# Optimization experiments

Measured on AMD Instinct MI355X. Metric: run time of the kernel, lower is better.

The kernel has to match this reference:

```python
import jax, jax.numpy as jnp
import numpy as np

N_ATOMS = 100000
N_EDGES = 6400000

def setup_inputs() -> dict:
    key = jax.random.key(0)
    k1, k2, k3 = jax.random.split(key, 3)
    R = jax.random.normal(k1, (N_ATOMS, 3), dtype=jnp.float32)
    idx_i = jax.random.randint(k2, (N_EDGES,), 0, N_ATOMS, dtype=jnp.int64)
    idx_j = jax.random.randint(k3, (N_EDGES,), 0, N_ATOMS, dtype=jnp.int64)
    return {"R": R, "idx_i": idx_i, "idx_j": idx_j}

def reference(R, idx_i, idx_j):
    # Gather coordinates at both ends of each edge, subtract, L2 norm over xyz.
    Rij = R[idx_i] - R[idx_j]            # [E, 3]
    d_ij = jnp.sqrt(jnp.sum(Rij * Rij, axis=-1))  # [E]
    return d_ij
```

## Files before the change

kernel.cpp:

```cpp
#include <hip/hip_runtime.h>
#include <hip/hip_bf16.h>


typedef int   v4i __attribute__((ext_vector_type(4)));
typedef float v4f __attribute__((ext_vector_type(4)));

__global__ __launch_bounds__(256) void pad_R_kernel(
    const float* __restrict__ R, float* __restrict__ R4, int n_atoms)
{
    const int i = blockIdx.x * blockDim.x + threadIdx.x;
    if (i < n_atoms) {
        const float x = R[3 * i + 0];
        const float y = R[3 * i + 1];
        const float z = R[3 * i + 2];
        v4f v = {x, y, z, 0.0f};
        *(v4f*)(R4 + 4 * (size_t)i) = v;
    }
}

__global__ __launch_bounds__(256) void pairwise_dist_kernel(
    const float* __restrict__ R4,
    const int* __restrict__ idx_i,
    const int* __restrict__ idx_j,
    float* __restrict__ out,
    int n_quads)
{
    const int quad = blockIdx.x * blockDim.x + threadIdx.x;
    if (quad >= n_quads) return;

    const v4i a = __builtin_nontemporal_load((const v4i*)idx_i + quad);
    const v4i b = __builtin_nontemporal_load((const v4i*)idx_j + quad);

    const v4f pa0 = __builtin_nontemporal_load((const v4f*)(R4 + 4 * (size_t)a.x));
    const v4f pb0 = __builtin_nontemporal_load((const v4f*)(R4 + 4 * (size_t)b.x));
    const v4f pa1 = __builtin_nontemporal_load((const v4f*)(R4 + 4 * (size_t)a.y));
    const v4f pb1 = __builtin_nontemporal_load((const v4f*)(R4 + 4 * (size_t)b.y));
    const v4f pa2 = __builtin_nontemporal_load((const v4f*)(R4 + 4 * (size_t)a.z));
    const v4f pb2 = __builtin_nontemporal_load((const v4f*)(R4 + 4 * (size_t)b.z));
    const v4f pa3 = __builtin_nontemporal_load((const v4f*)(R4 + 4 * (size_t)a.w));
    const v4f pb3 = __builtin_nontemporal_load((const v4f*)(R4 + 4 * (size_t)b.w));

    v4f o;
    {
        const v4f d = pa0 - pb0;
        o.x = sqrtf(d.x * d.x + d.y * d.y + d.z * d.z);
    }
    {
        const v4f d = pa1 - pb1;
        o.y = sqrtf(d.x * d.x + d.y * d.y + d.z * d.z);
    }
    {
        const v4f d = pa2 - pb2;
        o.z = sqrtf(d.x * d.x + d.y * d.y + d.z * d.z);
    }
    {
        const v4f d = pa3 - pb3;
        o.w = sqrtf(d.x * d.x + d.y * d.y + d.z * d.z);
    }
    __builtin_nontemporal_store(o, (v4f*)out + quad);
}

__global__ __launch_bounds__(64) void pairwise_dist_tail_kernel(
    const float* __restrict__ R4,
    const int* __restrict__ idx_i,
    const int* __restrict__ idx_j,
    float* __restrict__ out,
    int start, int n_edges)
{
    const int e = start + blockIdx.x * blockDim.x + threadIdx.x;
    if (e < n_edges) {
        const v4f pa = *(const v4f*)(R4 + 4 * (size_t)idx_i[e]);
        const v4f pb = *(const v4f*)(R4 + 4 * (size_t)idx_j[e]);
        const v4f d = pa - pb;
        out[e] = sqrtf(d.x * d.x + d.y * d.y + d.z * d.z);
    }
}

extern "C" void kernel_launch(void* const* d_in, const int* in_sizes, int n_in,
                              void* d_out, int out_size, void* d_ws, size_t ws_size,
                              hipStream_t stream)
{
    const float* R     = (const float*)d_in[0];
    const int*   idx_i = (const int*)d_in[1];
    const int*   idx_j = (const int*)d_in[2];
    float*       out   = (float*)d_out;

    const int n_atoms = in_sizes[0] / 3;
    const int n_edges = in_sizes[1];
    float*    R4      = (float*)d_ws;

    {
        const int block = 256;
        const int grid  = (n_atoms + block - 1) / block;
        pad_R_kernel<<<grid, block, 0, stream>>>(R, R4, n_atoms);
    }

    const int n_quads = n_edges >> 2;
    {
        const int block = 256;
        const int grid  = (n_quads + block - 1) / block;
        pairwise_dist_kernel<<<grid, block, 0, stream>>>(R4, idx_i, idx_j, out, n_quads);
    }

    const int tail_start = n_quads << 2;
    if (tail_start < n_edges) {
        const int tail = n_edges - tail_start;
        pairwise_dist_tail_kernel<<<(tail + 63) / 64, 64, 0, stream>>>(
            R4, idx_i, idx_j, out, tail_start, n_edges);
    }
}
```

Measured before the change: 159.5 us.

## Process eight edges per thread with inline-asm sc0 gathers and single wait

Each thread now handles eight edges instead of four, issuing sixteen coordinate gathers through inline global_load_dwordx4 with the sc0 cache-policy bit and then one explicit vmcnt(0) wait before computing distances. Index loads and output stores drop their nontemporal hints and become plain vector accesses. The aim is more memory-level parallelism per thread and keeping the small padded coordinate table cached rather than streamed. In exchange, register pressure rises, the thread count halves, and the hand-written asm hides the loads from compiler scheduling.

```diff
diff --git a/kernel.cpp b/kernel.cpp
--- a/kernel.cpp
+++ b/kernel.cpp
@@ -18,46 +18,67 @@
     }
 }
 
+__device__ __forceinline__ v4f gather_sc0(const float* base, int idx)
+{
+    v4f r;
+    const int voff = idx << 4;
+    asm volatile("global_load_dwordx4 %0, %1, %2 sc0"
+                 : "=v"(r)
+                 : "v"(voff), "s"(base)
+                 : "memory");
+    return r;
+}
+
+__device__ __forceinline__ float dist3(v4f a, v4f b)
+{
+    const v4f d = a - b;
+    return sqrtf(d.x * d.x + d.y * d.y + d.z * d.z);
+}
+
 __global__ __launch_bounds__(256) void pairwise_dist_kernel(
     const float* __restrict__ R4,
     const int* __restrict__ idx_i,
     const int* __restrict__ idx_j,
     float* __restrict__ out,
-    int n_quads)
+    int n_oct)
 {
-    const int quad = blockIdx.x * blockDim.x + threadIdx.x;
-    if (quad >= n_quads) return;
+    const int t = blockIdx.x * blockDim.x + threadIdx.x;
+    if (t >= n_oct) return;
 
-    const v4i a = __builtin_nontemporal_load((const v4i*)idx_i + quad);
-    const v4i b = __builtin_nontemporal_load((const v4i*)idx_j + quad);
+    const v4i a0 = ((const v4i*)idx_i)[2 * t + 0];
+    const v4i a1 = ((const v4i*)idx_i)[2 * t + 1];
+    const v4i b0 = ((const v4i*)idx_j)[2 * t + 0];
+    const v4i b1 = ((const v4i*)idx_j)[2 * t + 1];
 
-    const v4f pa0 = __builtin_nontemporal_load((const v4f*)(R4 + 4 * (size_t)a.x));
-    const v4f pb0 = __builtin_nontemporal_load((const v4f*)(R4 + 4 * (size_t)b.x));
-    const v4f pa1 = __builtin_nontemporal_load((const v4f*)(R4 + 4 * (size_t)a.y));
-    const v4f pb1 = __builtin_nontemporal_load((const v4f*)(R4 + 4 * (size_t)b.y));
-    const v4f pa2 = __builtin_nontemporal_load((const v4f*)(R4 + 4 * (size_t)a.z));
-    const v4f pb2 = __builtin_nontemporal_load((const v4f*)(R4 + 4 * (size_t)b.z));
-    const v4f pa3 = __builtin_nontemporal_load((const v4f*)(R4 + 4 * (size_t)a.w));
-    const v4f pb3 = __builtin_nontemporal_load((const v4f*)(R4 + 4 * (size_t)b.w));
+    v4f pa0 = gather_sc0(R4, a0.x), pb0 = gather_sc0(R4, b0.x);
+    v4f pa1 = gather_sc0(R4, a0.y), pb1 = gather_sc0(R4, b0.y);
+    v4f pa2 = gather_sc0(R4, a0.z), pb2 = gather_sc0(R4, b0.z);
+    v4f pa3 = gather_sc0(R4, a0.w), pb3 = gather_sc0(R4, b0.w);
+    v4f pa4 = gather_sc0(R4, a1.x), pb4 = gather_sc0(R4, b1.x);
+    v4f pa5 = gather_sc0(R4, a1.y), pb5 = gather_sc0(R4, b1.y);
+    v4f pa6 = gather_sc0(R4, a1.z), pb6 = gather_sc0(R4, b1.z);
+    v4f pa7 = gather_sc0(R4, a1.w), pb7 = gather_sc0(R4, b1.w);
 
-    v4f o;
-    {
-        const v4f d = pa0 - pb0;
-        o.x = sqrtf(d.x * d.x + d.y * d.y + d.z * d.z);
-    }
-    {
-        const v4f d = pa1 - pb1;
-        o.y = sqrtf(d.x * d.x + d.y * d.y + d.z * d.z);
-    }
-    {
-        const v4f d = pa2 - pb2;
-        o.z = sqrtf(d.x * d.x + d.y * d.y + d.z * d.z);
-    }
-    {
-        const v4f d = pa3 - pb3;
-        o.w = sqrtf(d.x * d.x + d.y * d.y + d.z * d.z);
-    }
-    __builtin_nontemporal_store(o, (v4f*)out + quad);
+    asm volatile("s_waitcnt vmcnt(0)"
+                 : "+v"(pa0), "+v"(pb0), "+v"(pa1), "+v"(pb1),
+                   "+v"(pa2), "+v"(pb2), "+v"(pa3), "+v"(pb3),
+                   "+v"(pa4), "+v"(pb4), "+v"(pa5), "+v"(pb5),
+                   "+v"(pa6), "+v"(pb6), "+v"(pa7), "+v"(pb7)
+                 :
+                 : "memory");
+
+    v4f o0, o1;
+    o0.x = dist3(pa0, pb0);
+    o0.y = dist3(pa1, pb1);
+    o0.z = dist3(pa2, pb2);
+    o0.w = dist3(pa3, pb3);
+    o1.x = dist3(pa4, pb4);
+    o1.y = dist3(pa5, pb5);
+    o1.z = dist3(pa6, pb6);
+    o1.w = dist3(pa7, pb7);
+
+    ((v4f*)out)[2 * t + 0] = o0;
+    ((v4f*)out)[2 * t + 1] = o1;
 }
 
 __global__ __launch_bounds__(64) void pairwise_dist_tail_kernel(
@@ -71,8 +92,7 @@
     if (e < n_edges) {
         const v4f pa = *(const v4f*)(R4 + 4 * (size_t)idx_i[e]);
         const v4f pb = *(const v4f*)(R4 + 4 * (size_t)idx_j[e]);
-        const v4f d = pa - pb;
-        out[e] = sqrtf(d.x * d.x + d.y * d.y + d.z * d.z);
+        out[e] = dist3(pa, pb);
     }
 }
 
@@ -95,14 +115,14 @@
         pad_R_kernel<<<grid, block, 0, stream>>>(R, R4, n_atoms);
     }
 
-    const int n_quads = n_edges >> 2;
+    const int n_oct = n_edges >> 3;
     {
         const int block = 256;
-        const int grid  = (n_quads + block - 1) / block;
-        pairwise_dist_kernel<<<grid, block, 0, stream>>>(R4, idx_i, idx_j, out, n_quads);
+        const int grid  = (n_oct + block - 1) / block;
+        pairwise_dist_kernel<<<grid, block, 0, stream>>>(R4, idx_i, idx_j, out, n_oct);
     }
 
-    const int tail_start = n_quads << 2;
+    const int tail_start = n_oct << 3;
     if (tail_start < n_edges) {
         const int tail = n_edges - tail_start;
         pairwise_dist_tail_kernel<<<(tail + 63) / 64, 64, 0, stream>>>(
```

After: 145.1 us. 9.1% less time.
